# Kernel optimization log

Measured on AMD Instinct MI355X. Metric: run time of the kernel, lower is better.

The kernel has to match this reference:

```python
import jax, jax.numpy as jnp
import numpy as np

INPUT, HIDDEN, OUT = 784, 64, 10
N_TEST = 10000
WVEC = INPUT * HIDDEN + HIDDEN + HIDDEN * OUT + OUT  # 50890
B = 64


def setup_inputs() -> dict:
    key = jax.random.key(0)
    k1, k2, k3, k4, k5 = jax.random.split(key, 5)
    inp1 = jax.random.normal(k1, (B, WVEC), dtype=jnp.float32)
    tar1 = jax.random.normal(k2, (B, WVEC), dtype=jnp.float32)
    inp2 = jax.random.normal(k3, (B, WVEC), dtype=jnp.float32)
    tar2 = jax.random.randint(k4, (B, N_TEST), 0, OUT, dtype=jnp.int64)
    images = jax.random.uniform(k5, (N_TEST, INPUT), dtype=jnp.float32)
    return {"inp1": inp1, "tar1": tar1, "inp2": inp2, "tar2": tar2, "images": images}


def _split_weights(w):
    # w: [B, 50890] -> W1 [B,H,I], B1 [B,H], W2 [B,O,H], B2 [B,O]
    b = w.shape[0]
    o1 = INPUT * HIDDEN
    o2 = o1 + HIDDEN
    o3 = o2 + HIDDEN * OUT
    W1 = w[:, :o1].reshape(b, HIDDEN, INPUT)
    B1 = w[:, o1:o2]
    W2 = w[:, o2:o3].reshape(b, OUT, HIDDEN)
    B2 = w[:, o3:]
    return W1, B1, W2, B2


def reference(inp1, tar1, inp2, tar2, images):
    # loss1: MSE * 20
    loss1 = 20.0 * jnp.mean(jnp.square(inp1 - tar1))
    # loss2: per-sample weight-conditioned MLP over fixed dataset, cross entropy
    W1, B1, W2, B2 = _split_weights(inp2)
    h = jax.nn.relu(jnp.einsum('nd,bhd->bnh', images, W1) + B1[:, None, :])   # [B,N,H]
    logits = jnp.einsum('bnh,boh->bno', h, W2) + B2[:, None, :]               # [B,N,O]
    logp = jax.nn.log_softmax(logits, axis=-1)
    ce = -jnp.take_along_axis(logp, tar2[..., None], axis=-1).squeeze(-1)     # [B,N]
    loss2 = jnp.mean(ce)  # mean over images per sample, then mean over batch
    combined = loss1 + loss2
    return (combined, loss1, loss2)
```

## Files before the change

### kernel.cpp

```cpp
#include <hip/hip_runtime.h>
#include <hip/hip_bf16.h>
#include <stdint.h>

#define INPUT_D 784
#define HIDDEN  64
#define OUTC    10
#define NTEST   10000
#define WVEC    50890
#define NBATCH  64
#define O1      50176
#define O2      50240
#define O3      50880
#define KPAD8   896
#define MPAD    10240
#define MTILES  80
#define NCOLS   4096
#define KTILES  7
#define H2      136
#define PREP_ROWS (MPAD + NCOLS)
#define L1_BLOCKS 512
#define SCALE1  0x7F7F7F7Fu

typedef __attribute__((ext_vector_type(8))) short  short8;
typedef __attribute__((ext_vector_type(4))) float  floatx4;
typedef __attribute__((ext_vector_type(4))) int    int4v;
typedef __attribute__((ext_vector_type(8))) int    int8v;

__device__ inline void async_copy16(const void* g, void* lds) {
  __builtin_amdgcn_global_load_lds(
      (const __attribute__((address_space(1))) void*)g,
      (__attribute__((address_space(3))) void*)lds, 16, 0, 0);
}

__global__ void prep_kernel(const float* __restrict__ img, const float* __restrict__ inp2,
                            const float* __restrict__ l1a, const float* __restrict__ l1b,
                            uint8_t* __restrict__ outI, uint8_t* __restrict__ outW,
                            float* __restrict__ accum) {
  const int blk = blockIdx.x;
  if (blk < PREP_ROWS) {
    const int c = threadIdx.x * 4;
    if (c >= KPAD8) return;
    const float* src;
    uint8_t* dst;
    bool valid;
    if (blk < MPAD) {
      valid = (blk < NTEST);
      src = img + (size_t)blk * INPUT_D;
      dst = outI + (size_t)blk * KPAD8;
    } else {
      const int rr = blk - MPAD;
      valid = true;
      src = inp2 + (size_t)(rr >> 6) * WVEC + (rr & 63) * INPUT_D;
      dst = outW + (size_t)rr * KPAD8;
    }
    float4 v = make_float4(0.f, 0.f, 0.f, 0.f);
    if (valid && (c + 4) <= INPUT_D) v = *(const float4*)(src + c);
    uint32_t w = 0;
    w = __builtin_amdgcn_cvt_pk_fp8_f32(v.x, v.y, w, false);
    w = __builtin_amdgcn_cvt_pk_fp8_f32(v.z, v.w, w, true);
    *(uint32_t*)(dst + c) = w;
  } else {
    const int n4 = (NBATCH * WVEC) / 4;
    const float4* A4 = (const float4*)l1a;
    const float4* B4 = (const float4*)l1b;
    float s = 0.f;
    for (int i = (blk - PREP_ROWS) * blockDim.x + threadIdx.x; i < n4;
         i += L1_BLOCKS * blockDim.x) {
      float4 x = A4[i], y = B4[i];
      float d0 = x.x - y.x, d1 = x.y - y.y, d2 = x.z - y.z, d3 = x.w - y.w;
      s += d0 * d0 + d1 * d1 + d2 * d2 + d3 * d3;
    }
    for (int off = 32; off; off >>= 1) s += __shfl_down(s, off);
    __shared__ float r[4];
    if ((threadIdx.x & 63) == 0) r[threadIdx.x >> 6] = s;
    __syncthreads();
    if (threadIdx.x == 0) atomicAdd(accum, r[0] + r[1] + r[2] + r[3]);
  }
}

__global__ __launch_bounds__(256)
void gemm_fused(const uint8_t* __restrict__ A,
                const uint8_t* __restrict__ Bm,
                const float* __restrict__ inp2,
                const int* __restrict__ tar2,
                float* __restrict__ accums) {
  __shared__ __align__(16) char smem[40032];
  uint8_t* Alds = (uint8_t*)smem;
  uint8_t* Blds = (uint8_t*)(smem + 16384);
  __hip_bfloat16* hlds  = (__hip_bfloat16*)smem;
  __hip_bfloat16* w2lds = (__hip_bfloat16*)(smem + 34816);
  float*          B2s   = (float*)(smem + 38912);
  int*            tars  = (int*)(smem + 38992);
  float*          red   = (float*)(smem + 40016);

  const int tid  = threadIdx.x;
  const int lane = tid & 63;
  const int wave = tid >> 6;
  const int wr   = (wave >> 1) * 64;
  const int wc   = (wave & 1) * 64;
  const int row0 = blockIdx.x * 128;
  const int col0 = blockIdx.y * 128;
  const int bbase = col0 >> 6;

  floatx4 acc[4][4];
#pragma unroll
  for (int i = 0; i < 4; ++i)
#pragma unroll
    for (int j = 0; j < 4; ++j) acc[i][j] = (floatx4){0.f, 0.f, 0.f, 0.f};

  const int lr   = lane >> 3;
  const int lcB  = (((lane & 7) ^ lr) * 16);
  const int sxor = lane & 7;
  const int q    = lane >> 4;
  const int c0   = (2 * q) ^ sxor;
  const int c1   = c0 ^ 1;

  for (int kt = 0; kt < KTILES; ++kt) {
    const int k0 = kt * 128;
#pragma unroll
    for (int c = 0; c < 4; ++c) {
      const int ch = wave * 4 + c;
      async_copy16(A  + (size_t)(row0 + ch * 8 + lr) * KPAD8 + k0 + lcB, Alds + ch * 1024);
      async_copy16(Bm + (size_t)(col0 + ch * 8 + lr) * KPAD8 + k0 + lcB, Blds + ch * 1024);
    }
    __syncthreads();
    int8v a8[4], b8[4];
#pragma unroll
    for (int mi = 0; mi < 4; ++mi) {
      const uint8_t* base = Alds + (wr + mi * 16 + (lane & 15)) * 128;
      int4v lo = *(const int4v*)(base + c0 * 16);
      int4v hi = *(const int4v*)(base + c1 * 16);
      a8[mi] = (int8v){lo.x, lo.y, lo.z, lo.w, hi.x, hi.y, hi.z, hi.w};
    }
#pragma unroll
    for (int ni = 0; ni < 4; ++ni) {
      const uint8_t* base = Blds + (wc + ni * 16 + (lane & 15)) * 128;
      int4v lo = *(const int4v*)(base + c0 * 16);
      int4v hi = *(const int4v*)(base + c1 * 16);
      b8[ni] = (int8v){lo.x, lo.y, lo.z, lo.w, hi.x, hi.y, hi.z, hi.w};
    }
#pragma unroll
    for (int mi = 0; mi < 4; ++mi)
#pragma unroll
      for (int ni = 0; ni < 4; ++ni)
        acc[mi][ni] = __builtin_amdgcn_mfma_scale_f32_16x16x128_f8f6f4(
            a8[mi], b8[ni], acc[mi][ni], 0 , 0 ,
            0, SCALE1, 0, SCALE1);
    __syncthreads();
  }

  for (int i = tid; i < 2048; i += 256) {
    const int bi = i >> 10, rem = i & 1023;
    const int o = rem >> 6, k = rem & 63;
    float v = (o < OUTC) ? inp2[(size_t)(bbase + bi) * WVEC + O2 + o * HIDDEN + k] : 0.f;
    w2lds[i] = __float2bfloat16(v);
  }
  if (tid < 20) B2s[tid] = inp2[(size_t)(bbase + tid / 10) * WVEC + O3 + tid % 10];
  {
    const int bi = tid >> 7, m = tid & 127;
    const int sample = row0 + m;
    tars[tid] = (sample < NTEST) ? tar2[(size_t)(bbase + bi) * NTEST + sample] : 0;
  }
#pragma unroll
  for (int ni = 0; ni < 4; ++ni) {
    const int n = wc + ni * 16 + (lane & 15);
    const float b1 = inp2[(size_t)(bbase + (n >> 6)) * WVEC + O1 + (n & 63)];
#pragma unroll
    for (int mi = 0; mi < 4; ++mi) {
      const int m = wr + mi * 16 + q * 4;
#pragma unroll
      for (int r = 0; r < 4; ++r) {
        float v = acc[mi][ni][r] + b1;
        hlds[(size_t)(m + r) * H2 + n] = __float2bfloat16(v > 0.f ? v : 0.f);
      }
    }
  }
  __syncthreads();

  const int col = lane & 15;
  float celocal = 0.f;
#pragma unroll
  for (int i = 0; i < 4; ++i) {
    const int task = wave * 4 + i;
    const int mt = task & 7;
    const int bi = task >> 3;
    short8 af0 = *(const short8*)&hlds[(size_t)(mt * 16 + col) * H2 + bi * 64 + q * 8];
    short8 af1 = *(const short8*)&hlds[(size_t)(mt * 16 + col) * H2 + bi * 64 + 32 + q * 8];
    short8 bf0 = *(const short8*)&w2lds[(bi * 16 + col) * 64 + q * 8];
    short8 bf1 = *(const short8*)&w2lds[(bi * 16 + col) * 64 + 32 + q * 8];
    floatx4 lacc = (floatx4){0.f, 0.f, 0.f, 0.f};
    lacc = __builtin_amdgcn_mfma_f32_16x16x32_bf16(af0, bf0, lacc, 0, 0, 0);
    lacc = __builtin_amdgcn_mfma_f32_16x16x32_bf16(af1, bf1, lacc, 0, 0, 0);
    const float b2 = (col < OUTC) ? B2s[bi * OUTC + col] : 0.f;
#pragma unroll
    for (int r = 0; r < 4; ++r) {
      float lv = (col < OUTC) ? (lacc[r] + b2) : -1e30f;
      float mx = lv;
      mx = fmaxf(mx, __shfl_xor(mx, 1));
      mx = fmaxf(mx, __shfl_xor(mx, 2));
      mx = fmaxf(mx, __shfl_xor(mx, 4));
      mx = fmaxf(mx, __shfl_xor(mx, 8));
      float ex = __expf(lv - mx);
      float sm = ex;
      sm += __shfl_xor(sm, 1);
      sm += __shfl_xor(sm, 2);
      sm += __shfl_xor(sm, 4);
      sm += __shfl_xor(sm, 8);
      const float lse = mx + __logf(sm);
      const int row = mt * 16 + q * 4 + r;
      const int tar = tars[bi * 128 + row];
      if (col == tar && (row0 + row) < NTEST) celocal += (lse - lv);
    }
  }
  for (int off = 32; off; off >>= 1) celocal += __shfl_down(celocal, off);
  if (lane == 0) red[wave] = celocal;
  __syncthreads();
  if (tid == 0) atomicAdd(&accums[1], red[0] + red[1] + red[2] + red[3]);
}

__global__ void finalize(const float* __restrict__ accums, float* __restrict__ out) {
  const float l1 = 20.f * accums[0] / (float)(NBATCH * WVEC);
  const float l2 = accums[1] / (float)(NBATCH * NTEST);
  out[0] = l1 + l2;
  out[1] = l1;
  out[2] = l2;
}

__global__ void loss1_fb(const float* __restrict__ a, const float* __restrict__ b,
                         float* __restrict__ accum) {
  const int n4 = (NBATCH * WVEC) / 4;
  const float4* A4 = (const float4*)a;
  const float4* B4 = (const float4*)b;
  float s = 0.f;
  for (int i = blockIdx.x * blockDim.x + threadIdx.x; i < n4; i += gridDim.x * blockDim.x) {
    float4 x = A4[i], y = B4[i];
    float d0 = x.x - y.x, d1 = x.y - y.y, d2 = x.z - y.z, d3 = x.w - y.w;
    s += d0 * d0 + d1 * d1 + d2 * d2 + d3 * d3;
  }
  for (int off = 32; off; off >>= 1) s += __shfl_down(s, off);
  __shared__ float r[4];
  if ((threadIdx.x & 63) == 0) r[threadIdx.x >> 6] = s;
  __syncthreads();
  if (threadIdx.x == 0) atomicAdd(accum, r[0] + r[1] + r[2] + r[3]);
}

__global__ void naive_ce(const float* __restrict__ inp2, const int* __restrict__ tar2,
                         const float* __restrict__ images, float* __restrict__ accum) {
  const int id = blockIdx.x * blockDim.x + threadIdx.x;
  float ce = 0.f;
  if (id < NBATCH * NTEST) {
    const int b = id / NTEST, n = id % NTEST;
    const float* w = inp2 + (size_t)b * WVEC;
    const float* im = images + (size_t)n * INPUT_D;
    float h[HIDDEN];
    for (int hh = 0; hh < HIDDEN; ++hh) {
      float s = w[O1 + hh];
      for (int d = 0; d < INPUT_D; ++d) s = fmaf(im[d], w[hh * INPUT_D + d], s);
      h[hh] = s > 0.f ? s : 0.f;
    }
    float mx = -1e30f, lg[OUTC];
    for (int o = 0; o < OUTC; ++o) {
      float s = w[O3 + o];
      for (int hh = 0; hh < HIDDEN; ++hh) s = fmaf(h[hh], w[O2 + o * HIDDEN + hh], s);
      lg[o] = s;
      mx = fmaxf(mx, s);
    }
    float sm = 0.f;
    for (int o = 0; o < OUTC; ++o) sm += __expf(lg[o] - mx);
    const float lse = mx + __logf(sm);
    const int t = tar2[(size_t)b * NTEST + n];
    float lt = lg[0];
    for (int o = 1; o < OUTC; ++o) lt = (o == t) ? lg[o] : lt;
    ce = lse - lt;
  }
  for (int off = 32; off; off >>= 1) ce += __shfl_down(ce, off);
  __shared__ float r[4];
  if ((threadIdx.x & 63) == 0) r[threadIdx.x >> 6] = ce;
  __syncthreads();
  if (threadIdx.x == 0) atomicAdd(accum, r[0] + r[1] + r[2] + r[3]);
}

extern "C" void kernel_launch(void* const* d_in, const int* in_sizes, int n_in,
                              void* d_out, int out_size, void* d_ws, size_t ws_size,
                              hipStream_t stream) {
  const float* inp1   = (const float*)d_in[0];
  const float* tar1   = (const float*)d_in[1];
  const float* inp2   = (const float*)d_in[2];
  const int*   tar2   = (const int*)d_in[3];
  const float* images = (const float*)d_in[4];
  float*       out    = (float*)d_out;

  const size_t img_bytes  = (size_t)MPAD * KPAD8;
  const size_t wall_bytes = (size_t)NCOLS * KPAD8;
  const size_t needed     = 256 + img_bytes + wall_bytes;

  if (ws_size >= needed) {
    float* accums = (float*)d_ws;
    uint8_t* imgb = (uint8_t*)d_ws + 256;
    uint8_t* wall = (uint8_t*)d_ws + 256 + img_bytes;
    hipMemsetAsync(d_ws, 0, 256, stream);
    prep_kernel<<<PREP_ROWS + L1_BLOCKS, 256, 0, stream>>>(images, inp2, inp1, tar1,
                                                           imgb, wall, accums);
    gemm_fused<<<dim3(MTILES, 32), 256, 0, stream>>>(imgb, wall, inp2, tar2, accums);
    finalize<<<1, 1, 0, stream>>>(accums, out);
  } else {
    hipMemsetAsync(d_out, 0, 3 * sizeof(float), stream);
    loss1_fb<<<1024, 256, 0, stream>>>(inp1, tar1, out + 1);
    naive_ce<<<(NBATCH * NTEST + 255) / 256, 256, 0, stream>>>(inp2, tar2, images, out + 2);
    finalize<<<1, 1, 0, stream>>>(out + 1, out);
  }
}
```

Measured before the change: 183.4 us.

## Double-buffer LDS tiles in FP8 GEMM and grid-stride the prep kernel

The GEMM main loop now uses two LDS buffers for the A and B tiles. It issues the async global-to-LDS copy for the next K tile right after the barrier, so memory traffic overlaps the MFMA work on the current tile and one barrier per iteration is removed. A fragments are now loaded per row-block inside the MFMA loop to ease register pressure. The prep kernel switches from one block per row plus separate MSE blocks to a fixed 1024-block grid-stride loop, where each thread does FP8 casting and then the MSE reduction. The larger 64KB LDS allocation may lower the number of resident blocks per CU, and the per-element division adds integer cost in prep.

```diff
diff --git a/kernel.cpp b/kernel.cpp
--- a/kernel.cpp
+++ b/kernel.cpp
@@ -17,9 +17,9 @@
 #define NCOLS   4096
 #define KTILES  7
 #define H2      136
-#define PREP_ROWS (MPAD + NCOLS)
-#define L1_BLOCKS 512
 #define SCALE1  0x7F7F7F7Fu
+#define CAST_ROWS (MPAD + NCOLS)
+#define CAST_GROUPS (CAST_ROWS * (KPAD8/4))
 
 typedef __attribute__((ext_vector_type(8))) short  short8;
 typedef __attribute__((ext_vector_type(4))) float  floatx4;
@@ -36,19 +36,20 @@
                             const float* __restrict__ l1a, const float* __restrict__ l1b,
                             uint8_t* __restrict__ outI, uint8_t* __restrict__ outW,
                             float* __restrict__ accum) {
-  const int blk = blockIdx.x;
-  if (blk < PREP_ROWS) {
-    const int c = threadIdx.x * 4;
-    if (c >= KPAD8) return;
+  const int gtid = blockIdx.x * blockDim.x + threadIdx.x;
+  const int nthr = gridDim.x * blockDim.x;
+  for (int i = gtid; i < CAST_GROUPS; i += nthr) {
+    const int row = i / 224;
+    const int c   = (i - row * 224) * 4;
     const float* src;
     uint8_t* dst;
     bool valid;
-    if (blk < MPAD) {
-      valid = (blk < NTEST);
-      src = img + (size_t)blk * INPUT_D;
-      dst = outI + (size_t)blk * KPAD8;
+    if (row < MPAD) {
+      valid = (row < NTEST);
+      src = img + (size_t)row * INPUT_D;
+      dst = outI + (size_t)row * KPAD8;
     } else {
-      const int rr = blk - MPAD;
+      const int rr = row - MPAD;
       valid = true;
       src = inp2 + (size_t)(rr >> 6) * WVEC + (rr & 63) * INPUT_D;
       dst = outW + (size_t)rr * KPAD8;
@@ -59,23 +60,21 @@
     w = __builtin_amdgcn_cvt_pk_fp8_f32(v.x, v.y, w, false);
     w = __builtin_amdgcn_cvt_pk_fp8_f32(v.z, v.w, w, true);
     *(uint32_t*)(dst + c) = w;
-  } else {
-    const int n4 = (NBATCH * WVEC) / 4;
-    const float4* A4 = (const float4*)l1a;
-    const float4* B4 = (const float4*)l1b;
-    float s = 0.f;
-    for (int i = (blk - PREP_ROWS) * blockDim.x + threadIdx.x; i < n4;
-         i += L1_BLOCKS * blockDim.x) {
-      float4 x = A4[i], y = B4[i];
-      float d0 = x.x - y.x, d1 = x.y - y.y, d2 = x.z - y.z, d3 = x.w - y.w;
-      s += d0 * d0 + d1 * d1 + d2 * d2 + d3 * d3;
-    }
-    for (int off = 32; off; off >>= 1) s += __shfl_down(s, off);
-    __shared__ float r[4];
-    if ((threadIdx.x & 63) == 0) r[threadIdx.x >> 6] = s;
-    __syncthreads();
-    if (threadIdx.x == 0) atomicAdd(accum, r[0] + r[1] + r[2] + r[3]);
-  }
+  }
+  const int n4 = (NBATCH * WVEC) / 4;
+  const float4* A4 = (const float4*)l1a;
+  const float4* B4 = (const float4*)l1b;
+  float s = 0.f;
+  for (int i = gtid; i < n4; i += nthr) {
+    float4 x = A4[i], y = B4[i];
+    float d0 = x.x - y.x, d1 = x.y - y.y, d2 = x.z - y.z, d3 = x.w - y.w;
+    s += d0 * d0 + d1 * d1 + d2 * d2 + d3 * d3;
+  }
+  for (int off = 32; off; off >>= 1) s += __shfl_down(s, off);
+  __shared__ float r[4];
+  if ((threadIdx.x & 63) == 0) r[threadIdx.x >> 6] = s;
+  __syncthreads();
+  if (threadIdx.x == 0) atomicAdd(accum, r[0] + r[1] + r[2] + r[3]);
 }
 
 __global__ __launch_bounds__(256)
@@ -84,9 +83,9 @@
                 const float* __restrict__ inp2,
                 const int* __restrict__ tar2,
                 float* __restrict__ accums) {
-  __shared__ __align__(16) char smem[40032];
-  uint8_t* Alds = (uint8_t*)smem;
-  uint8_t* Blds = (uint8_t*)(smem + 16384);
+  __shared__ __align__(16) char smem[65536];
+  uint8_t* Abuf[2] = {(uint8_t*)smem,           (uint8_t*)(smem + 32768)};
+  uint8_t* Bbuf[2] = {(uint8_t*)(smem + 16384), (uint8_t*)(smem + 49152)};
   __hip_bfloat16* hlds  = (__hip_bfloat16*)smem;
   __hip_bfloat16* w2lds = (__hip_bfloat16*)(smem + 34816);
   float*          B2s   = (float*)(smem + 38912);
@@ -115,39 +114,50 @@
   const int c0   = (2 * q) ^ sxor;
   const int c1   = c0 ^ 1;
 
+  const uint8_t* Ag = A  + (size_t)(row0 + wave * 32 + lr) * KPAD8 + lcB;
+  const uint8_t* Bg = Bm + (size_t)(col0 + wave * 32 + lr) * KPAD8 + lcB;
+
+#pragma unroll
+  for (int c = 0; c < 4; ++c) {
+    async_copy16(Ag + (size_t)(c * 8) * KPAD8, Abuf[0] + (wave * 4 + c) * 1024);
+    async_copy16(Bg + (size_t)(c * 8) * KPAD8, Bbuf[0] + (wave * 4 + c) * 1024);
+  }
+
+#pragma unroll
   for (int kt = 0; kt < KTILES; ++kt) {
-    const int k0 = kt * 128;
-#pragma unroll
-    for (int c = 0; c < 4; ++c) {
-      const int ch = wave * 4 + c;
-      async_copy16(A  + (size_t)(row0 + ch * 8 + lr) * KPAD8 + k0 + lcB, Alds + ch * 1024);
-      async_copy16(Bm + (size_t)(col0 + ch * 8 + lr) * KPAD8 + k0 + lcB, Blds + ch * 1024);
-    }
     __syncthreads();
-    int8v a8[4], b8[4];
-#pragma unroll
-    for (int mi = 0; mi < 4; ++mi) {
-      const uint8_t* base = Alds + (wr + mi * 16 + (lane & 15)) * 128;
-      int4v lo = *(const int4v*)(base + c0 * 16);
-      int4v hi = *(const int4v*)(base + c1 * 16);
-      a8[mi] = (int8v){lo.x, lo.y, lo.z, lo.w, hi.x, hi.y, hi.z, hi.w};
-    }
+    if (kt + 1 < KTILES) {
+      const int k0 = (kt + 1) * 128;
+#pragma unroll
+      for (int c = 0; c < 4; ++c) {
+        async_copy16(Ag + (size_t)(c * 8) * KPAD8 + k0, Abuf[(kt + 1) & 1] + (wave * 4 + c) * 1024);
+        async_copy16(Bg + (size_t)(c * 8) * KPAD8 + k0, Bbuf[(kt + 1) & 1] + (wave * 4 + c) * 1024);
+      }
+    }
+    const uint8_t* Asrc = Abuf[kt & 1];
+    const uint8_t* Bsrc = Bbuf[kt & 1];
+    int8v b8[4];
 #pragma unroll
     for (int ni = 0; ni < 4; ++ni) {
-      const uint8_t* base = Blds + (wc + ni * 16 + (lane & 15)) * 128;
+      const uint8_t* base = Bsrc + (wc + ni * 16 + (lane & 15)) * 128;
       int4v lo = *(const int4v*)(base + c0 * 16);
       int4v hi = *(const int4v*)(base + c1 * 16);
       b8[ni] = (int8v){lo.x, lo.y, lo.z, lo.w, hi.x, hi.y, hi.z, hi.w};
     }
 #pragma unroll
-    for (int mi = 0; mi < 4; ++mi)
+    for (int mi = 0; mi < 4; ++mi) {
+      const uint8_t* base = Asrc + (wr + mi * 16 + (lane & 15)) * 128;
+      int4v lo = *(const int4v*)(base + c0 * 16);
+      int4v hi = *(const int4v*)(base + c1 * 16);
+      int8v a8 = (int8v){lo.x, lo.y, lo.z, lo.w, hi.x, hi.y, hi.z, hi.w};
 #pragma unroll
       for (int ni = 0; ni < 4; ++ni)
         acc[mi][ni] = __builtin_amdgcn_mfma_scale_f32_16x16x128_f8f6f4(
-            a8[mi], b8[ni], acc[mi][ni], 0 , 0 ,
+            a8, b8[ni], acc[mi][ni], 0 , 0 ,
             0, SCALE1, 0, SCALE1);
-    __syncthreads();
-  }
+    }
+  }
+  __syncthreads();
 
   for (int i = tid; i < 2048; i += 256) {
     const int bi = i >> 10, rem = i & 1023;
@@ -299,8 +309,7 @@
     uint8_t* imgb = (uint8_t*)d_ws + 256;
     uint8_t* wall = (uint8_t*)d_ws + 256 + img_bytes;
     hipMemsetAsync(d_ws, 0, 256, stream);
-    prep_kernel<<<PREP_ROWS + L1_BLOCKS, 256, 0, stream>>>(images, inp2, inp1, tar1,
-                                                           imgb, wall, accums);
+    prep_kernel<<<1024, 256, 0, stream>>>(images, inp2, inp1, tar1, imgb, wall, accums);
     gemm_fused<<<dim3(MTILES, 32), 256, 0, stream>>>(imgb, wall, inp2, tar2, accums);
     finalize<<<1, 1, 0, stream>>>(accums, out);
   } else {
```

New measurement: 194.5 us. +6.1%, slower.
